# Optimization experiments

Hardware: AMD Instinct MI355X
Metric: run time of the kernel (lower is better)

## Reference

```python
import jax, jax.numpy as jnp
import numpy as np
from jax import lax

B, D, H, W = 4, 64, 64, 64
CH = 150


def setup_inputs() -> dict:
    key = jax.random.key(0)
    k1, k2, k3, k4 = jax.random.split(key, 4)
    image = jax.random.uniform(k1, (B, 2, D, H, W), dtype=jnp.float32)
    # PyTorch-like init scales
    h_w = jax.random.normal(k2, (CH, 1, 3, 3, 3), dtype=jnp.float32) * (1.0 / np.sqrt(27.0))
    h_b = jax.random.normal(k3, (CH,), dtype=jnp.float32) * 0.05
    p_w = jax.random.normal(k4, (1, CH, 1, 1, 1), dtype=jnp.float32) * (1.0 / np.sqrt(CH))
    return {"image": image, "h_w": h_w, "h_b": h_b, "p_w": p_w, "k": 30}


def _max_pool3(v):
    # 3x3x3 max pool, stride 1, padding 1 (torch pads with -inf for max pool)
    return lax.reduce_window(
        v, -jnp.inf, lax.max,
        window_dimensions=(1, 1, 3, 3, 3),
        window_strides=(1, 1, 1, 1, 1),
        padding=[(0, 0), (0, 0), (1, 1), (1, 1), (1, 1)])


def reference(image, h_w, h_b, p_w, k):
    x = image[:, 0:1]            # [B,1,D,H,W] occupancy
    r = image[:, 1:2]            # [B,1,D,H,W] reward
    h = lax.conv_general_dilated(
        x, h_w, window_strides=(1, 1, 1), padding="SAME",
        dimension_numbers=("NCDHW", "OIDHW", "NCDHW"))
    h = jax.nn.relu(h + h_b[None, :, None, None, None])  # [B,150,D,H,W]
    # 1x1x1 conv == channel contraction
    p = jax.nn.sigmoid(jnp.einsum("bcdhw,c->bdhw", h, p_w[0, :, 0, 0, 0])[:, None])
    v = r
    for _ in range(k):
        v = jnp.maximum(v, r + p * (_max_pool3(v) - r))
    return v
```

## Files before the change

kernel.cpp:

```cpp
#include <hip/hip_runtime.h>
#include <math.h>

#define NEG_INF (-__builtin_inff())

typedef __attribute__((ext_vector_type(8))) short short8;
typedef __attribute__((ext_vector_type(4))) float f32x4;

__device__ __forceinline__ unsigned f2bf(float f) {
    union { float f; unsigned u; } v; v.f = f;
    return (v.u + 0x7fffu + ((v.u >> 16) & 1u)) >> 16;
}

__device__ __forceinline__ float dpp_shr1(float x) {
    return __int_as_float(__builtin_amdgcn_update_dpp(
        0, __float_as_int(x), 0x111, 0xF, 0xF, true));
}
__device__ __forceinline__ float dpp_shr2(float x) {
    return __int_as_float(__builtin_amdgcn_update_dpp(
        0, __float_as_int(x), 0x112, 0xF, 0xF, true));
}
__device__ __forceinline__ float dpp_shr4(float x) {
    return __int_as_float(__builtin_amdgcn_update_dpp(
        0, __float_as_int(x), 0x114, 0xF, 0xF, true));
}
__device__ __forceinline__ float dpp_shr8(float x) {
    return __int_as_float(__builtin_amdgcn_update_dpp(
        0, __float_as_int(x), 0x118, 0xF, 0xF, true));
}
__device__ __forceinline__ float dpp_shl1(float x) {
    return __int_as_float(__builtin_amdgcn_update_dpp(
        0, __float_as_int(x), 0x101, 0xF, 0xF, true));
}

__global__ __launch_bounds__(256) void pad_kernel(
    const float* __restrict__ img, unsigned short* __restrict__ pad)
{
    int i = blockIdx.x * 256 + threadIdx.x;
    if (i >= 66 * 66 * 66) return;
    int b = blockIdx.y;
    int z = i / 4356;
    int rem = i - z * 4356;
    int y = rem / 66;
    int x = rem - y * 66;
    float v = 0.f;
    if (z >= 1 && z <= 64 && y >= 1 && y <= 64 && x >= 1 && x <= 64)
        v = img[((size_t)b << 19) + ((z - 1) << 12) + ((y - 1) << 6) + (x - 1)];
    pad[(size_t)b * 287496 + i] = (unsigned short)f2bf(v);
}

__global__ __launch_bounds__(256, 4) void gate_mfma(
    const unsigned short* __restrict__ pad,
    const float* __restrict__ hw, const float* __restrict__ hb,
    const float* __restrict__ pw, float* __restrict__ p)
{
    __shared__ int4 Bsh[10 * 64];

    const int lane = threadIdx.x & 63;
    const int col  = lane & 15;
    const int q    = lane >> 4;
    const int wid  = threadIdx.x >> 6;
    const int W    = blockIdx.x * 4 + wid;

    for (int t = wid; t < 10; t += 4) {
        int c = 16 * t + col;
        bool cv = c < 150;
        unsigned hv[8];
        #pragma unroll
        for (int j = 0; j < 8; ++j) {
            int k = 8 * q + j;
            float wv = 0.f;
            if (cv) {
                if (k < 27) wv = hw[c * 27 + k];
                else if (k == 27) wv = hb[c];
            }
            hv[j] = f2bf(wv);
        }
        Bsh[t * 64 + lane] = make_int4(hv[0] | (hv[1] << 16), hv[2] | (hv[3] << 16),
                                       hv[4] | (hv[5] << 16), hv[6] | (hv[7] << 16));
    }
    float pwv[10];
    #pragma unroll
    for (int t = 0; t < 10; ++t) {
        int c = 16 * t + col;
        pwv[t] = (c < 150) ? pw[c] : 0.f;
    }
    __syncthreads();

    int4 bfrag[10];
    #pragma unroll
    for (int t = 0; t < 10; ++t) bfrag[t] = Bsh[t * 64 + lane];

    int offL[8]; unsigned cstA[8]; bool ldA[8];
    #pragma unroll
    for (int j = 0; j < 8; ++j) {
        int k = 8 * q + j;
        int dz = (k * 57) >> 9;
        int rem = k - 9 * dz;
        int dy = (rem * 171) >> 9;
        int dx = rem - 3 * dy;
        ldA[j]  = (k < 27);
        offL[j] = (k < 27) ? (dz * 4356 + dy * 66 + dx) : 0;
        cstA[j] = (k == 27) ? 0x3F80u : 0u;
    }

    int y = W & 63, zz = (W >> 6) & 63, b = W >> 12;
    int rbase = b * 287496 + zz * 4356 + y * 66 + col;

    #pragma unroll 2
    for (int i = 0; i < 4; ++i) {
        int x0    = i << 4;
        int abase = rbase + x0;

        unsigned av[8];
        #pragma unroll
        for (int j = 0; j < 8; ++j) {
            unsigned v = pad[abase + offL[j]];
            av[j] = ldA[j] ? v : cstA[j];
        }
        union { int4 i4; short8 s8; } af, bfu;
        af.i4 = make_int4(av[0] | (av[1] << 16), av[2] | (av[3] << 16),
                          av[4] | (av[5] << 16), av[6] | (av[7] << 16));

        const f32x4 zero = {0.f, 0.f, 0.f, 0.f};
        f32x4 rr[10];
        #pragma unroll
        for (int t = 0; t < 10; ++t) {
            bfu.i4 = bfrag[t];
            rr[t] = __builtin_amdgcn_mfma_f32_16x16x32_bf16(af.s8, bfu.s8, zero, 0, 0, 0);
        }
        float ax = 0.f, ay = 0.f, az = 0.f, aw = 0.f;
        #pragma unroll
        for (int t = 0; t < 10; ++t) {
            ax = fmaf(pwv[t], fmaxf(rr[t].x, 0.f), ax);
            ay = fmaf(pwv[t], fmaxf(rr[t].y, 0.f), ay);
            az = fmaf(pwv[t], fmaxf(rr[t].z, 0.f), az);
            aw = fmaf(pwv[t], fmaxf(rr[t].w, 0.f), aw);
        }
        ax += dpp_shr1(ax); ax += dpp_shr2(ax); ax += dpp_shr4(ax); ax += dpp_shr8(ax);
        ay += dpp_shr1(ay); ay += dpp_shr2(ay); ay += dpp_shr4(ay); ay += dpp_shr8(ay);
        az += dpp_shr1(az); az += dpp_shr2(az); az += dpp_shr4(az); az += dpp_shr8(az);
        aw += dpp_shr1(aw); aw += dpp_shr2(aw); aw += dpp_shr4(aw); aw += dpp_shr8(aw);
        if (col == 15) {
            float4 o;
            o.x = 1.f / (1.f + __expf(-ax));
            o.y = 1.f / (1.f + __expf(-ay));
            o.z = 1.f / (1.f + __expf(-az));
            o.w = 1.f / (1.f + __expf(-aw));
            *(float4*)(p + (b << 18) + (zz << 12) + (y << 6) + x0 + 4 * q) = o;
        }
    }
}

#define YC 16
#define PL 1024

template<int T>
__global__ __launch_bounds__(512, 4) void prop_kernel(
    const float* __restrict__ vin, int sstride,
    const float* __restrict__ rimg,
    const float* __restrict__ pbuf,
    float* __restrict__ vout)
{
    __shared__ float TL[10 * PL];
    __shared__ float VEX[2 * PL];

    int blk = blockIdx.x;
    int b  = blk >> 7;
    int tz = ((blk >> 3) & 15) << 2;
    int ty = (blk & 7) << 3;

    const float* vb = vin  + (size_t)b * sstride;
    const float* rb = rimg + ((size_t)b << 19);
    const float* pb = pbuf + ((size_t)b << 18);
    float*       ob = vout + ((size_t)b << 18);

    int tid  = threadIdx.x;
    int x4   = tid & 15, x0 = x4 << 2;
    int yy   = (tid >> 4) & 15;
    int h    = tid >> 8;

    int gy = ty + yy - 4;
    bool vy = (unsigned)gy < 64u;
    int lbase = yy * 64 + x0;
    int goff  = gy * 64 + x0;

    float4 v[6];
    #pragma unroll
    for (int zi = 0; zi < 6; ++zi) {
        int z  = h ? (11 - zi) : zi;
        int gz = tz + z - 4;
        float4 val = make_float4(NEG_INF, NEG_INF, NEG_INF, NEG_INF);
        if (vy && ((unsigned)gz < 64u)) val = *(const float4*)(vb + (gz << 12) + goff);
        v[zi] = val;
    }
    *(float4*)(VEX + h * PL + lbase) = v[5];
    __syncthreads();

    #pragma unroll
    for (int it = 0; it < T; ++it) {
        const int lo = 5 - T + it;
        bool act_t = (yy >= lo - 1) && (yy < 17 - lo);
        bool act   = (yy >= lo) && (yy < YC - lo);

        float4 vexN = *(const float4*)(VEX + (h ^ 1) * PL + lbase);
        float4 t[5];
        #pragma unroll
        for (int zi = lo; zi < 6; ++zi) {
            float4 za = v[zi - 1];
            float4 zb = v[zi];
            float4 zc = (zi == 5) ? vexN : v[zi + 1];
            float4 zm;
            zm.x = fmaxf(fmaxf(za.x, zb.x), zc.x);
            zm.y = fmaxf(fmaxf(za.y, zb.y), zc.y);
            zm.z = fmaxf(fmaxf(za.z, zb.z), zc.z);
            zm.w = fmaxf(fmaxf(za.w, zb.w), zc.w);
            float lm = dpp_shr1(zm.w);
            float rm = dpp_shl1(zm.x);
            if (x4 == 0)  lm = NEG_INF;
            if (x4 == 15) rm = NEG_INF;
            float4 tt;
            tt.x = fmaxf(lm, fmaxf(zm.x, zm.y));
            tt.y = fmaxf(zm.x, fmaxf(zm.y, zm.z));
            tt.z = fmaxf(zm.y, fmaxf(zm.z, zm.w));
            tt.w = fmaxf(fmaxf(zm.z, zm.w), rm);
            t[zi - lo] = tt;
            int z = h ? (11 - zi) : zi;
            if (act_t) *(float4*)(TL + (z - 1) * PL + lbase) = tt;
        }
        __syncthreads();

        #pragma unroll
        for (int zi = lo; zi < 6; ++zi) {
            int z  = h ? (11 - zi) : zi;
            int gz = tz + z - 4;
            if (act) {
                const float* tp = TL + (z - 1) * PL + lbase;
                float4 tu = *(const float4*)(tp - 64);
                float4 td = *(const float4*)(tp + 64);
                float4 ts = t[zi - lo];
                float4 m3;
                m3.x = fmaxf(fmaxf(tu.x, td.x), ts.x);
                m3.y = fmaxf(fmaxf(tu.y, td.y), ts.y);
                m3.z = fmaxf(fmaxf(tu.z, td.z), ts.z);
                m3.w = fmaxf(fmaxf(tu.w, td.w), ts.w);
                if (vy && ((unsigned)gz < 64u)) {
                    int off = (gz << 12) + goff;
                    float4 pv = *(const float4*)(pb + off);
                    float4 rv = *(const float4*)(rb + off);
                    float4 nv;
                    nv.x = fmaxf(v[zi].x, fmaf(pv.x, m3.x - rv.x, rv.x));
                    nv.y = fmaxf(v[zi].y, fmaf(pv.y, m3.y - rv.y, rv.y));
                    nv.z = fmaxf(v[zi].z, fmaf(pv.z, m3.z - rv.z, rv.z));
                    nv.w = fmaxf(v[zi].w, fmaf(pv.w, m3.w - rv.w, rv.w));
                    v[zi] = nv;
                    if (it == T - 1) *(float4*)(ob + off) = nv;
                }
            }
        }
        *(float4*)(VEX + h * PL + lbase) = v[5];
        __syncthreads();
    }
}

extern "C" void kernel_launch(void* const* d_in, const int* in_sizes, int n_in,
                              void* d_out, int out_size, void* d_ws, size_t ws_size,
                              hipStream_t stream) {
    const float* img = (const float*)d_in[0];
    const float* hw  = (const float*)d_in[1];
    const float* hb  = (const float*)d_in[2];
    const float* pw  = (const float*)d_in[3];

    float* out = (float*)d_out;
    float* p   = (float*)d_ws;
    float* vA  = (float*)((char*)d_ws + (4u << 20));
    unsigned short* pad = (unsigned short*)((char*)d_ws + (4u << 20));

    pad_kernel<<<dim3(1124, 4), 256, 0, stream>>>(img, pad);
    gate_mfma<<<4096, 256, 0, stream>>>(pad, hw, hb, pw, p);

    const float* r0 = img + (1 << 18);

    prop_kernel<4><<<512, 512, 0, stream>>>(r0,  1 << 19, r0, p, vA);
    prop_kernel<4><<<512, 512, 0, stream>>>(vA,  1 << 18, r0, p, out);
    prop_kernel<4><<<512, 512, 0, stream>>>(out, 1 << 18, r0, p, vA);
    prop_kernel<4><<<512, 512, 0, stream>>>(vA,  1 << 18, r0, p, out);
    prop_kernel<4><<<512, 512, 0, stream>>>(out, 1 << 18, r0, p, vA);
    prop_kernel<4><<<512, 512, 0, stream>>>(vA,  1 << 18, r0, p, out);
    prop_kernel<4><<<512, 512, 0, stream>>>(out, 1 << 18, r0, p, vA);
    prop_kernel<2><<<512, 512, 0, stream>>>(vA,  1 << 18, r0, p, out);
}
```

Baseline: 179.4 us.

## Size prop halo by temporal depth and split final iterations into two T=3 passes

The propagation kernel's tile and halo size (YC, PL, z planes) now depend on the template parameter T, so shallower passes use smaller halos, fewer threads and less shared memory. Block indices are remapped so consecutive workgroups are spread across the index space, likely for XCD/cache locality. The last two launches (4+2 iterations) become two 3-iteration launches with 448 threads. The aim is to cut redundant halo computation and loads per launch, at the cost of a different launch mix and thread count.

Measured after the change: 173.0 us (median of 2 runs). -3.6%, faster.

```diff
diff --git a/kernel.cpp b/kernel.cpp
--- a/kernel.cpp
+++ b/kernel.cpp
@@ -151,9 +151,6 @@
     }
 }
 
-#define YC 16
-#define PL 1024
-
 template<int T>
 __global__ __launch_bounds__(512, 4) void prop_kernel(
     const float* __restrict__ vin, int sstride,
@@ -161,10 +158,15 @@
     const float* __restrict__ pbuf,
     float* __restrict__ vout)
 {
-    __shared__ float TL[10 * PL];
+    constexpr int YC = 8 + 2 * T;
+    constexpr int PL = 64 * YC;
+    constexpr int P  = 2 * T + 4;
+    constexpr int HF = T + 2;
+    __shared__ float TL[(P - 2) * PL];
     __shared__ float VEX[2 * PL];
 
-    int blk = blockIdx.x;
+    int hwb = blockIdx.x;
+    int blk = (hwb & 7) * 64 + (hwb >> 3);
     int b  = blk >> 7;
     int tz = ((blk >> 3) & 15) << 2;
     int ty = (blk & 7) << 3;
@@ -175,40 +177,41 @@
     float*       ob = vout + ((size_t)b << 18);
 
     int tid  = threadIdx.x;
-    int x4   = tid & 15, x0 = x4 << 2;
-    int yy   = (tid >> 4) & 15;
-    int h    = tid >> 8;
-
-    int gy = ty + yy - 4;
+    int h    = (tid >= 16 * YC);
+    int t2   = tid - h * 16 * YC;
+    int x4   = t2 & 15, x0 = x4 << 2;
+    int yy   = t2 >> 4;
+
+    int gy = ty + yy - T;
     bool vy = (unsigned)gy < 64u;
     int lbase = yy * 64 + x0;
     int goff  = gy * 64 + x0;
 
-    float4 v[6];
-    #pragma unroll
-    for (int zi = 0; zi < 6; ++zi) {
-        int z  = h ? (11 - zi) : zi;
-        int gz = tz + z - 4;
+    float4 v[HF];
+    #pragma unroll
+    for (int zi = 0; zi < HF; ++zi) {
+        int z  = h ? (P - 1 - zi) : zi;
+        int gz = tz + z - T;
         float4 val = make_float4(NEG_INF, NEG_INF, NEG_INF, NEG_INF);
         if (vy && ((unsigned)gz < 64u)) val = *(const float4*)(vb + (gz << 12) + goff);
         v[zi] = val;
     }
-    *(float4*)(VEX + h * PL + lbase) = v[5];
+    *(float4*)(VEX + h * PL + lbase) = v[HF - 1];
     __syncthreads();
 
     #pragma unroll
     for (int it = 0; it < T; ++it) {
-        const int lo = 5 - T + it;
-        bool act_t = (yy >= lo - 1) && (yy < 17 - lo);
+        const int lo = 1 + it;
+        bool act_t = (yy >= lo - 1) && (yy < YC - lo + 1);
         bool act   = (yy >= lo) && (yy < YC - lo);
 
         float4 vexN = *(const float4*)(VEX + (h ^ 1) * PL + lbase);
-        float4 t[5];
-        #pragma unroll
-        for (int zi = lo; zi < 6; ++zi) {
+        float4 t[T + 1];
+        #pragma unroll
+        for (int zi = lo; zi < HF; ++zi) {
             float4 za = v[zi - 1];
             float4 zb = v[zi];
-            float4 zc = (zi == 5) ? vexN : v[zi + 1];
+            float4 zc = (zi == HF - 1) ? vexN : v[zi + 1];
             float4 zm;
             zm.x = fmaxf(fmaxf(za.x, zb.x), zc.x);
             zm.y = fmaxf(fmaxf(za.y, zb.y), zc.y);
@@ -224,15 +227,15 @@
             tt.z = fmaxf(zm.y, fmaxf(zm.z, zm.w));
             tt.w = fmaxf(fmaxf(zm.z, zm.w), rm);
             t[zi - lo] = tt;
-            int z = h ? (11 - zi) : zi;
+            int z = h ? (P - 1 - zi) : zi;
             if (act_t) *(float4*)(TL + (z - 1) * PL + lbase) = tt;
         }
         __syncthreads();
 
         #pragma unroll
-        for (int zi = lo; zi < 6; ++zi) {
-            int z  = h ? (11 - zi) : zi;
-            int gz = tz + z - 4;
+        for (int zi = lo; zi < HF; ++zi) {
+            int z  = h ? (P - 1 - zi) : zi;
+            int gz = tz + z - T;
             if (act) {
                 const float* tp = TL + (z - 1) * PL + lbase;
                 float4 tu = *(const float4*)(tp - 64);
@@ -257,7 +260,7 @@
                 }
             }
         }
-        *(float4*)(VEX + h * PL + lbase) = v[5];
+        *(float4*)(VEX + h * PL + lbase) = v[HF - 1];
         __syncthreads();
     }
 }
@@ -286,6 +289,6 @@
     prop_kernel<4><<<512, 512, 0, stream>>>(vA,  1 << 18, r0, p, out);
     prop_kernel<4><<<512, 512, 0, stream>>>(out, 1 << 18, r0, p, vA);
     prop_kernel<4><<<512, 512, 0, stream>>>(vA,  1 << 18, r0, p, out);
-    prop_kernel<4><<<512, 512, 0, stream>>>(out, 1 << 18, r0, p, vA);
-    prop_kernel<2><<<512, 512, 0, stream>>>(vA,  1 << 18, r0, p, out);
-}
+    prop_kernel<3><<<512, 448, 0, stream>>>(out, 1 << 18, r0, p, vA);
+    prop_kernel<3><<<512, 448, 0, stream>>>(vA,  1 << 18, r0, p, out);
+}
```
